# Kernel tuning notes

Hardware: AMD Instinct MI355X
Metric: run time of the kernel (lower is better)

Reference implementation:

```python
import jax, jax.numpy as jnp
import numpy as np

H, W, D = 480, 640, 128
K = 17
R = K // 2
TEMPORAL_LENGTH = 1.0
CHUNK = 1024


def setup_inputs() -> dict:
    key = jax.random.key(0)
    ks = jax.random.split(key, 9)
    N = 500_000
    M = 65_536
    t = jax.random.uniform(ks[0], (N,), jnp.float32)
    y = jax.random.randint(ks[1], (N,), 0, H)
    x = jax.random.randint(ks[2], (N,), 0, W)
    query_y = jax.random.randint(ks[3], (M,), 0, H)
    query_x = jax.random.randint(ks[4], (M,), 0, W)
    query_t = jax.random.uniform(ks[5], (M,), jnp.float32)
    T = jax.random.normal(ks[6], (1, D), jnp.float32) * 25.0
    X = jax.random.normal(ks[7], (1, D), jnp.float32) * 25.0
    Y = jax.random.normal(ks[8], (1, D), jnp.float32) * 25.0
    return dict(t=t, y=y, x=x, query_y=query_y, query_x=query_x,
                query_t=query_t, T=T, X=X, Y=Y)


def _kernel_weights(X, Y):
    # (K*K, D) complex weights: exp(i*(norm_dx*X + norm_dy*Y))
    r = jnp.arange(-R, R + 1, dtype=jnp.float32)
    dy, dx = jnp.meshgrid(r, r, indexing='ij')
    phase = (dx / R)[..., None] * X[0] + (dy / R)[..., None] * Y[0]  # (K,K,D)
    return jnp.exp(1j * phase).reshape(K * K, D)


def reference(t, y, x, query_y, query_x, query_t, T, X, Y):
    kw = _kernel_weights(X, Y)                       # (K*K, D) complex64
    # temporal embedding + scatter-add into flat grid
    t_norm = t / TEMPORAL_LENGTH
    temp_emb = jnp.exp(1j * (t_norm[:, None] * T[0][None, :]))  # (N, D)
    flat_idx = y * W + x                                         # (N,)
    grid = jnp.zeros((H * W, D), jnp.complex64).at[flat_idx].add(temp_emb)
    counts = jnp.zeros((H * W,), jnp.float32).at[flat_idx].add(1.0)
    grid = grid.reshape(H, W, D)
    counts = counts.reshape(H, W)
    # zero-pad by radius
    pg = jnp.pad(grid, ((R, R), (R, R), (0, 0)))
    pc = jnp.pad(counts, ((R, R), (R, R)))
    # flattened window offsets (row-major, matching torch loop order)
    off = jnp.arange(-R, R + 1)
    oy, ox = jnp.meshgrid(off, off, indexing='ij')
    oy = oy.reshape(-1)
    ox = ox.reshape(-1)                               # (K*K,)
    qy = (query_y + R).reshape(-1, CHUNK)
    qx = (query_x + R).reshape(-1, CHUNK)
    M = query_y.shape[0]

    def chunk_fn(q):
        cy, cx = q
        iy = cy[:, None] + oy[None, :]                # (CHUNK, K*K)
        ix = cx[:, None] + ox[None, :]
        feat = pg[iy, ix]                             # (CHUNK, K*K, D)
        cnt = pc[iy, ix]                              # (CHUNK, K*K)
        emb = jnp.einsum('qkd,kd->qd', feat, kw)      # weighted window reduce
        return emb, cnt.sum(axis=1)

    emb_c, cnt_c = jax.lax.map(chunk_fn, (qy, qx))
    out_emb = emb_c.reshape(M, D)
    out_cnt = cnt_c.reshape(M)
    # re-center by query time
    recen = jnp.exp(-1j * ((query_t / TEMPORAL_LENGTH)[:, None] * T[0][None, :]))
    out_emb = out_emb * recen
    return out_emb / jnp.maximum(out_cnt, 1.0)[:, None]
```

## Files before the change

### kernel.cpp

```cpp
#include <hip/hip_runtime.h>
#include <hip/hip_fp16.h>
#include <math.h>

#define HH 480
#define WW 640
#define RAD 8
#define KK 17
#define DD 128
#define HWPIX (HH*WW)
#define NBLK (HWPIX/256)
#define TS 160
#define XT 4

static inline size_t al256(size_t x){ return (x + 255) & ~(size_t)255; }

__global__ void hist_kernel(const int* __restrict__ cy, const int* __restrict__ cx,
                            unsigned* __restrict__ off, int N) {
    int e = blockIdx.x*blockDim.x + threadIdx.x;
    if (e >= N) return;
    atomicAdd(&off[cy[e]*WW + cx[e]], 1u);
}

__global__ void scan1_kernel(unsigned* __restrict__ off, unsigned* __restrict__ bs) {
    __shared__ unsigned sh[256];
    int t = threadIdx.x, b = blockIdx.x;
    unsigned v = off[b*256 + t];
    sh[t] = v; __syncthreads();
    for (int st = 1; st < 256; st <<= 1) {
        unsigned a = (t >= st) ? sh[t-st] : 0u;
        __syncthreads();
        sh[t] += a;
        __syncthreads();
    }
    off[b*256 + t] = sh[t] - v;
    if (t == 255) bs[b] = sh[255];
}

__global__ void scan2_kernel(unsigned* __restrict__ bs) {
    __shared__ unsigned sh[256];
    __shared__ unsigned carry;
    int t = threadIdx.x;
    if (t == 0) carry = 0u;
    __syncthreads();
    for (int base = 0; base < NBLK; base += 256) {
        int i = base + t;
        unsigned v = (i < NBLK) ? bs[i] : 0u;
        sh[t] = v; __syncthreads();
        for (int st = 1; st < 256; st <<= 1) {
            unsigned a = (t >= st) ? sh[t-st] : 0u;
            __syncthreads();
            sh[t] += a;
            __syncthreads();
        }
        unsigned tot = sh[255];
        if (i < NBLK) bs[i] = (sh[t] - v) + carry;
        __syncthreads();
        if (t == 0) carry += tot;
        __syncthreads();
    }
}

__global__ void scan3_kernel(unsigned* __restrict__ off, const unsigned* __restrict__ bs) {
    int i = blockIdx.x*256 + threadIdx.x;
    off[i] += bs[blockIdx.x];
}

__global__ void sort_kernel(const int* __restrict__ ey, const int* __restrict__ ex,
                            const float* __restrict__ t, unsigned* __restrict__ off,
                            float* __restrict__ tss, int* __restrict__ xs, int N) {
    int e = blockIdx.x*blockDim.x + threadIdx.x;
    if (e >= N) return;
    int pix = ey[e]*WW + ex[e];
    unsigned pos = atomicAdd(&off[pix], 1u);
    tss[pos] = t[e];
    xs[pos]  = ex[e];
}

__global__ void qsort_kernel(const int* __restrict__ qy, const int* __restrict__ qx,
                             unsigned* __restrict__ qoff, unsigned* __restrict__ qidx, int M) {
    int q = blockIdx.x*blockDim.x + threadIdx.x;
    if (q >= M) return;
    int pix = qy[q]*WW + qx[q];
    unsigned pos = atomicAdd(&qoff[pix], 1u);
    qidx[pos] = q;
}

__global__ void qcnt_kernel(const int* __restrict__ qy, const int* __restrict__ qx,
                            const unsigned* __restrict__ off, float* __restrict__ qcnt, int M) {
    int q = blockIdx.x*blockDim.x + threadIdx.x;
    if (q >= M) return;
    int cy = qy[q], cx = qx[q];
    int xlo = cx - RAD; if (xlo < 0) xlo = 0;
    int xhi = cx + RAD; if (xhi > WW-1) xhi = WW-1;
    unsigned s = 0;
    for (int i = 0; i < KK; ++i) {
        int yy = cy + i - RAD;
        if ((unsigned)yy >= HH) continue;
        int plo = yy*WW + xlo, phi = yy*WW + xhi;
        unsigned st = plo ? off[plo-1] : 0u;
        s += off[phi] - st;
    }
    qcnt[q] = (float)s;
}

__global__ __launch_bounds__(128) void rowsweep_kernel(
        const unsigned* __restrict__ off, const float* __restrict__ tss,
        const float* __restrict__ Tw, const float* __restrict__ Xw,
        __half2* __restrict__ Hout, int rb0) {
    __shared__ float ringr[KK][DD];
    __shared__ float ringi[KK][DD];
    int dd   = threadIdx.x;
    int hrow = blockIdx.y;
    int hy   = rb0 + hrow;
    int x0   = blockIdx.x * TS;
    int x1   = x0 + TS; if (x1 > WW) x1 = WW;
    __half2* hp = Hout + (long long)hrow*WW*DD + dd;

    if ((unsigned)hy >= HH) {
        __half2 z = __floats2half2_rn(0.f, 0.f);
        for (int x = x0; x < x1; ++x) hp[(long long)x*DD] = z;
        return;
    }

    float Td = Tw[dd];
    float th = Xw[dd] * 0.125f;
    float s, c;
    sincosf(th, &s, &c);
    const float er_ = c,  ei_ = s;
    const float ar  = c,  ai  = -s;
    sincosf(8.f*th, &s, &c);
    const float w0r = c,  w0i = -s;
    sincosf(9.f*th, &s, &c);
    const float w17r = c, w17i = s;

    const int rowbase = hy*WW;
    const unsigned* offr = off + rowbase;

#define GAT(col, gr, gi)                                                    \
    {                                                                       \
        gr = 0.f; gi = 0.f;                                                 \
        if ((unsigned)(col) < WW) {                                         \
            int pix_ = rowbase + (col);                                     \
            unsigned st_ = pix_ ? off[pix_-1] : 0u;                         \
            unsigned en_ = offr[(col)];                                     \
            for (unsigned p_ = st_; p_ < en_; ++p_) {                       \
                float ss_, cc_;                                             \
                __sincosf(tss[p_]*Td, &ss_, &cc_);                          \
                gr += cc_; gi += ss_;                                       \
            }                                                               \
        }                                                                   \
    }

    float hr = 0.f, hi = 0.f;
    float wr = w0r, wi = w0i;
    #pragma unroll
    for (int j = 0; j < KK; ++j) {
        float gr, gi; GAT(x0 + j - RAD, gr, gi);
        hr = fmaf(gr, wr, hr); hr = fmaf(-gi, wi, hr);
        hi = fmaf(gr, wi, hi); hi = fmaf(gi, wr, hi);
        ringr[j][dd] = gr; ringi[j][dd] = gi;
        float nr = wr*er_ - wi*ei_;
        wi       = wr*ei_ + wi*er_;
        wr       = nr;
    }
    hp[(long long)x0*DD] = __floats2half2_rn(hr, hi);

    int ri = 0;
    for (int xn = x0 + 1; xn < x1; ++xn) {
        float gr, gi; GAT(xn + RAD, gr, gi);
        float gor = ringr[ri][dd], goi = ringi[ri][dd];
        ringr[ri][dd] = gr; ringi[ri][dd] = gi;
        ri = (ri + 1 == KK) ? 0 : ri + 1;
        float tr = hr - (gor*w0r - goi*w0i) + (gr*w17r - gi*w17i);
        float ti = hi - (gor*w0i + goi*w0r) + (gr*w17i + gi*w17r);
        hr = tr*ar - ti*ai;
        hi = tr*ai + ti*ar;
        hp[(long long)xn*DD] = __floats2half2_rn(hr, hi);
    }
#undef GAT
}

__global__ __launch_bounds__(256) void query_sep_kernel(
        const unsigned* __restrict__ qidx, const int* __restrict__ qy,
        const int* __restrict__ qx, const float* __restrict__ qt,
        const float* __restrict__ Tw, const float* __restrict__ Yw,
        const unsigned* __restrict__ H, const float* __restrict__ qcnt,
        float* __restrict__ out, int M, int r0, int band, int rb0,
        long long out_n, int real_only) {
    int lt   = threadIdx.x;
    int p    = blockIdx.x*4 + (lt >> 6);
    int lane = lt & 63;
    if (p >= M) return;
    int q = (int)qidx[p];
    int cy = qy[q];
    if (cy < r0 || cy >= r0 + band) return;
    int cx = qx[q];
    int d0 = lane*2, d1 = d0 + 1;

    float wyr0, wyi0, cst0, sst0, wyr1, wyi1, cst1, sst1;
    {
        float s, c;
        float Y0 = Yw[d0], Y1 = Yw[d1];
        sincosf(-Y0, &s, &c);        wyr0 = c; wyi0 = s;
        sincosf(Y0*0.125f, &sst0, &cst0);
        sincosf(-Y1, &s, &c);        wyr1 = c; wyi1 = s;
        sincosf(Y1*0.125f, &sst1, &cst1);
    }

    const unsigned* hp = H + ((long long)(cy - RAD - rb0)*WW + cx)*DD + d0;
    float er0 = 0.f, ei0 = 0.f, er1 = 0.f, ei1 = 0.f;
    #pragma unroll
    for (int i = 0; i < KK; ++i) {
        uint2 v = *(const uint2*)(hp + (long long)i*WW*DD);
        float2 f0 = __half22float2(*(const __half2*)&v.x);
        float2 f1 = __half22float2(*(const __half2*)&v.y);
        er0 = fmaf(f0.x, wyr0, er0); er0 = fmaf(-f0.y, wyi0, er0);
        ei0 = fmaf(f0.x, wyi0, ei0); ei0 = fmaf(f0.y, wyr0, ei0);
        er1 = fmaf(f1.x, wyr1, er1); er1 = fmaf(-f1.y, wyi1, er1);
        ei1 = fmaf(f1.x, wyi1, ei1); ei1 = fmaf(f1.y, wyr1, ei1);
        float nr;
        nr = wyr0*cst0 - wyi0*sst0; wyi0 = wyr0*sst0 + wyi0*cst0; wyr0 = nr;
        nr = wyr1*cst1 - wyi1*sst1; wyi1 = wyr1*sst1 + wyi1*cst1; wyr1 = nr;
    }

    float inv = 1.0f / fmaxf(qcnt[q], 1.0f);
    float s, c, qtv = qt[q];
    sincosf(qtv * Tw[d0], &s, &c);
    float outr0 = (er0*c + ei0*s) * inv, outi0 = (ei0*c - er0*s) * inv;
    sincosf(qtv * Tw[d1], &s, &c);
    float outr1 = (er1*c + ei1*s) * inv, outi1 = (ei1*c - er1*s) * inv;

    long long base = (long long)q*DD + d0;
    if (real_only) {
        if (base + 1 < out_n) *(float2*)(out + base) = make_float2(outr0, outr1);
        else if (base < out_n) out[base] = outr0;
    } else if (2*base + 3 < out_n) {
        *(float4*)(out + 2*base) = make_float4(outr0, outi0, outr1, outi1);
    }
}

__global__ __launch_bounds__(256) void query_direct_kernel(
        const int* __restrict__ qy, const int* __restrict__ qx,
        const float* __restrict__ qt, const float* __restrict__ Tw,
        const float* __restrict__ Xw, const float* __restrict__ Yw,
        const unsigned* __restrict__ off, const float* __restrict__ tss,
        const int* __restrict__ xs, float* __restrict__ out,
        int M, long long out_n, int real_only) {
    __shared__ float2 swx[KK*DD];
    __shared__ float2 swy[KK*DD];
    int lt = threadIdx.x;
    for (int idx = lt; idx < KK*DD; idx += 256) {
        int j = idx / DD, dd = idx & (DD-1);
        float s, c;
        sincosf((float)(j - RAD) * 0.125f * Xw[dd], &s, &c);
        swx[idx] = make_float2(c, s);
        sincosf((float)(j - RAD) * 0.125f * Yw[dd], &s, &c);
        swy[idx] = make_float2(c, s);
    }
    __syncthreads();

    int q = blockIdx.x*2 + (lt >> 7);
    int d = lt & (DD-1);
    if (q >= M) return;

    int cy = qy[q], cx = qx[q];
    float Td = Tw[d];
    int xlo = cx - RAD; if (xlo < 0) xlo = 0;
    int xhi = cx + RAD; if (xhi > WW-1) xhi = WW-1;

    float accr = 0.f, acci = 0.f;
    unsigned cnt = 0;
    for (int i = 0; i < KK; ++i) {
        int yy = cy + i - RAD;
        if ((unsigned)yy >= HH) continue;
        int plo = yy*WW + xlo, phi = yy*WW + xhi;
        unsigned st = plo ? off[plo-1] : 0u;
        unsigned en = off[phi];
        cnt += en - st;
        float rr = 0.f, ri = 0.f;
        for (unsigned p = st; p < en; ++p) {
            float te = tss[p];
            int   xe = xs[p];
            float2 wx = swx[(xe - cx + RAD)*DD + d];
            float s, c;
            __sincosf(te * Td, &s, &c);
            rr = fmaf(c, wx.x, rr); rr = fmaf(-s, wx.y, rr);
            ri = fmaf(c, wx.y, ri); ri = fmaf(s, wx.x, ri);
        }
        float2 wy = swy[i*DD + d];
        accr = fmaf(rr, wy.x, accr); accr = fmaf(-ri, wy.y, accr);
        acci = fmaf(rr, wy.y, acci); acci = fmaf(ri, wy.x, acci);
    }

    float s, c;
    sincosf(qt[q] * Td, &s, &c);
    float inv = 1.0f / fmaxf((float)cnt, 1.0f);
    float outr = (accr*c + acci*s) * inv;
    float outi = (acci*c - accr*s) * inv;
    long long base = (long long)q*DD + d;
    if (real_only) { if (base < out_n) out[base] = outr; }
    else if (2*base + 1 < out_n) { out[2*base] = outr; out[2*base+1] = outi; }
}

extern "C" void kernel_launch(void* const* d_in, const int* in_sizes, int n_in,
                              void* d_out, int out_size, void* d_ws, size_t ws_size,
                              hipStream_t stream) {
    const float* t  = (const float*)d_in[0];
    const int*   ey = (const int*)d_in[1];
    const int*   ex = (const int*)d_in[2];
    const int*   qy = (const int*)d_in[3];
    const int*   qx = (const int*)d_in[4];
    const float* qt = (const float*)d_in[5];
    const float* Tw = (const float*)d_in[6];
    const float* Xw = (const float*)d_in[7];
    const float* Yw = (const float*)d_in[8];

    int N = in_sizes[0];
    int M = in_sizes[3];

    size_t off_b  = al256((size_t)HWPIX*4);
    size_t qoff_b = al256((size_t)HWPIX*4);
    size_t bs_b   = al256((size_t)NBLK*4);
    size_t tss_b  = al256((size_t)N*4);
    size_t xs_b   = al256((size_t)N*4);
    size_t qidx_b = al256((size_t)M*4);
    size_t qc_b   = al256((size_t)M*4);
    size_t fixed  = off_b + qoff_b + bs_b + tss_b + xs_b + qidx_b + qc_b;
    size_t need_min = off_b + qoff_b + bs_b + tss_b + xs_b;

    if (ws_size < need_min || d_ws == nullptr) {
        hipMemsetAsync(d_out, 0, (size_t)out_size*4, stream);
        return;
    }

    char*     ws   = (char*)d_ws;
    unsigned* off  = (unsigned*)ws;
    unsigned* qoff = (unsigned*)(ws + off_b);
    unsigned* bs   = (unsigned*)(ws + off_b + qoff_b);
    float*    tss  = (float*)(ws + off_b + qoff_b + bs_b);
    int*      xs   = (int*)(ws + off_b + qoff_b + bs_b + tss_b);
    unsigned* qidx = (unsigned*)(ws + off_b + qoff_b + bs_b + tss_b + xs_b);
    float*    qcnt = (float*)(ws + off_b + qoff_b + bs_b + tss_b + xs_b + qidx_b);
    __half2*  H    = (__half2*)(ws + fixed);

    long long full = (long long)M * DD;
    int real_only = (out_size < 2*full) ? 1 : 0;

    hipMemsetAsync(off, 0, off_b + (size_t)HWPIX*4, stream);
    hist_kernel<<<(N+255)/256, 256, 0, stream>>>(ey, ex, off, N);
    scan1_kernel<<<NBLK, 256, 0, stream>>>(off, bs);
    scan2_kernel<<<1, 256, 0, stream>>>(bs);
    scan3_kernel<<<NBLK, 256, 0, stream>>>(off, bs);
    sort_kernel<<<(N+255)/256, 256, 0, stream>>>(ey, ex, t, off, tss, xs, N);

    long long band_sz = 0;
    if (ws_size > fixed) {
        long long hrows_fit = (long long)((ws_size - fixed) / ((size_t)WW*DD*4));
        band_sz = hrows_fit - 16;
        if (band_sz > HH) band_sz = HH;
    }

    if (band_sz < 32) {
        query_direct_kernel<<<(M+1)/2, 256, 0, stream>>>(
            qy, qx, qt, Tw, Xw, Yw, off, tss, xs, (float*)d_out,
            M, (long long)out_size, real_only);
        return;
    }

    qcnt_kernel<<<(M+255)/256, 256, 0, stream>>>(qy, qx, off, qcnt, M);

    hist_kernel<<<(M+255)/256, 256, 0, stream>>>(qy, qx, qoff, M);
    scan1_kernel<<<NBLK, 256, 0, stream>>>(qoff, bs);
    scan2_kernel<<<1, 256, 0, stream>>>(bs);
    scan3_kernel<<<NBLK, 256, 0, stream>>>(qoff, bs);
    qsort_kernel<<<(M+255)/256, 256, 0, stream>>>(qy, qx, qoff, qidx, M);

    for (int r0 = 0; r0 < HH; r0 += (int)band_sz) {
        int band  = (HH - r0 < band_sz) ? (HH - r0) : (int)band_sz;
        int hrows = band + 16;
        dim3 g(XT, hrows);
        rowsweep_kernel<<<g, 128, 0, stream>>>(off, tss, Tw, Xw, H, r0 - RAD);
        query_sep_kernel<<<(M+3)/4, 256, 0, stream>>>(
            qidx, qy, qx, qt, Tw, Yw, (const unsigned*)H, qcnt, (float*)d_out,
            M, r0, band, r0 - RAD, (long long)out_size, real_only);
    }
}
```

Baseline: 252.6 us.

## Batch histogram/scan kernels for events and queries, register ring, finer row tiles

Event and query histograms, prefix scans and the query sort/count step are merged into dual-purpose kernels, cutting the number of launches. The rowsweep kernel keeps its 17-entry ring buffer in registers through a fully unrolled loop instead of shared memory. It also carries the previous segment end forward instead of reloading the start offset per column. Tile width is halved (TS 80, XT 8) so more blocks run in parallel, at the cost of more redundant window-initialisation gathers per row.

```diff
diff --git a/kernel.cpp b/kernel.cpp
--- a/kernel.cpp
+++ b/kernel.cpp
@@ -9,22 +9,29 @@
 #define DD 128
 #define HWPIX (HH*WW)
 #define NBLK (HWPIX/256)
-#define TS 160
-#define XT 4
+#define TS 80
+#define XT 8
 
 static inline size_t al256(size_t x){ return (x + 255) & ~(size_t)255; }
 
-__global__ void hist_kernel(const int* __restrict__ cy, const int* __restrict__ cx,
-                            unsigned* __restrict__ off, int N) {
+__global__ void hist_dual_kernel(const int* __restrict__ ey, const int* __restrict__ ex, int N,
+                                 const int* __restrict__ qy, const int* __restrict__ qx, int M,
+                                 unsigned* __restrict__ off, unsigned* __restrict__ qoff) {
     int e = blockIdx.x*blockDim.x + threadIdx.x;
-    if (e >= N) return;
-    atomicAdd(&off[cy[e]*WW + cx[e]], 1u);
-}
-
-__global__ void scan1_kernel(unsigned* __restrict__ off, unsigned* __restrict__ bs) {
+    if (blockIdx.y == 0) {
+        if (e < N) atomicAdd(&off[ey[e]*WW + ex[e]], 1u);
+    } else {
+        if (e < M) atomicAdd(&qoff[qy[e]*WW + qx[e]], 1u);
+    }
+}
+
+__global__ void scan1_dual_kernel(unsigned* __restrict__ o0, unsigned* __restrict__ o1,
+                                  unsigned* __restrict__ bs) {
     __shared__ unsigned sh[256];
     int t = threadIdx.x, b = blockIdx.x;
-    unsigned v = off[b*256 + t];
+    unsigned* off = (b < NBLK) ? o0 : o1;
+    int bb = (b < NBLK) ? b : b - NBLK;
+    unsigned v = off[bb*256 + t];
     sh[t] = v; __syncthreads();
     for (int st = 1; st < 256; st <<= 1) {
         unsigned a = (t >= st) ? sh[t-st] : 0u;
@@ -32,13 +39,14 @@
         sh[t] += a;
         __syncthreads();
     }
-    off[b*256 + t] = sh[t] - v;
+    off[bb*256 + t] = sh[t] - v;
     if (t == 255) bs[b] = sh[255];
 }
 
-__global__ void scan2_kernel(unsigned* __restrict__ bs) {
+__global__ void scan2_dual_kernel(unsigned* __restrict__ bs_all) {
     __shared__ unsigned sh[256];
     __shared__ unsigned carry;
+    unsigned* bs = bs_all + blockIdx.x*NBLK;
     int t = threadIdx.x;
     if (t == 0) carry = 0u;
     __syncthreads();
@@ -60,9 +68,12 @@
     }
 }
 
-__global__ void scan3_kernel(unsigned* __restrict__ off, const unsigned* __restrict__ bs) {
-    int i = blockIdx.x*256 + threadIdx.x;
-    off[i] += bs[blockIdx.x];
+__global__ void scan3_dual_kernel(unsigned* __restrict__ o0, unsigned* __restrict__ o1,
+                                  const unsigned* __restrict__ bs) {
+    int b = blockIdx.x;
+    unsigned* off = (b < NBLK) ? o0 : o1;
+    int bb = (b < NBLK) ? b : b - NBLK;
+    off[bb*256 + threadIdx.x] += bs[b];
 }
 
 __global__ void sort_kernel(const int* __restrict__ ey, const int* __restrict__ ex,
@@ -76,20 +87,15 @@
     xs[pos]  = ex[e];
 }
 
-__global__ void qsort_kernel(const int* __restrict__ qy, const int* __restrict__ qx,
-                             unsigned* __restrict__ qoff, unsigned* __restrict__ qidx, int M) {
-    int q = blockIdx.x*blockDim.x + threadIdx.x;
-    if (q >= M) return;
-    int pix = qy[q]*WW + qx[q];
-    unsigned pos = atomicAdd(&qoff[pix], 1u);
-    qidx[pos] = q;
-}
-
-__global__ void qcnt_kernel(const int* __restrict__ qy, const int* __restrict__ qx,
-                            const unsigned* __restrict__ off, float* __restrict__ qcnt, int M) {
+__global__ void qsortcnt_kernel(const int* __restrict__ qy, const int* __restrict__ qx,
+                                unsigned* __restrict__ qoff, unsigned* __restrict__ qidx,
+                                const unsigned* __restrict__ off, float* __restrict__ qcnt, int M) {
     int q = blockIdx.x*blockDim.x + threadIdx.x;
     if (q >= M) return;
     int cy = qy[q], cx = qx[q];
+    int pix = cy*WW + cx;
+    unsigned pos = atomicAdd(&qoff[pix], 1u);
+    qidx[pos] = q;
     int xlo = cx - RAD; if (xlo < 0) xlo = 0;
     int xhi = cx + RAD; if (xhi > WW-1) xhi = WW-1;
     unsigned s = 0;
@@ -107,8 +113,6 @@
         const unsigned* __restrict__ off, const float* __restrict__ tss,
         const float* __restrict__ Tw, const float* __restrict__ Xw,
         __half2* __restrict__ Hout, int rb0) {
-    __shared__ float ringr[KK][DD];
-    __shared__ float ringi[KK][DD];
     int dd   = threadIdx.x;
     int hrow = blockIdx.y;
     int hy   = rb0 + hrow;
@@ -136,48 +140,58 @@
     const int rowbase = hy*WW;
     const unsigned* offr = off + rowbase;
 
-#define GAT(col, gr, gi)                                                    \
+    int cfirst = x0 - RAD; if (cfirst < 0) cfirst = 0;
+    int pix0 = rowbase + cfirst;
+    unsigned pen = pix0 ? off[pix0-1] : 0u;
+
+#define GATC(col, gr, gi)                                                   \
     {                                                                       \
         gr = 0.f; gi = 0.f;                                                 \
         if ((unsigned)(col) < WW) {                                         \
-            int pix_ = rowbase + (col);                                     \
-            unsigned st_ = pix_ ? off[pix_-1] : 0u;                         \
             unsigned en_ = offr[(col)];                                     \
-            for (unsigned p_ = st_; p_ < en_; ++p_) {                       \
+            for (unsigned p_ = pen; p_ < en_; ++p_) {                       \
                 float ss_, cc_;                                             \
                 __sincosf(tss[p_]*Td, &ss_, &cc_);                          \
                 gr += cc_; gi += ss_;                                       \
             }                                                               \
+            pen = en_;                                                      \
         }                                                                   \
     }
+
+    float ringr[KK], ringi[KK];
 
     float hr = 0.f, hi = 0.f;
     float wr = w0r, wi = w0i;
     #pragma unroll
     for (int j = 0; j < KK; ++j) {
-        float gr, gi; GAT(x0 + j - RAD, gr, gi);
+        float gr, gi; GATC(x0 + j - RAD, gr, gi);
         hr = fmaf(gr, wr, hr); hr = fmaf(-gi, wi, hr);
         hi = fmaf(gr, wi, hi); hi = fmaf(gi, wr, hi);
-        ringr[j][dd] = gr; ringi[j][dd] = gi;
+        ringr[j] = gr; ringi[j] = gi;
         float nr = wr*er_ - wi*ei_;
         wi       = wr*ei_ + wi*er_;
         wr       = nr;
     }
     hp[(long long)x0*DD] = __floats2half2_rn(hr, hi);
 
-    int ri = 0;
-    for (int xn = x0 + 1; xn < x1; ++xn) {
-        float gr, gi; GAT(xn + RAD, gr, gi);
-        float gor = ringr[ri][dd], goi = ringi[ri][dd];
-        ringr[ri][dd] = gr; ringi[ri][dd] = gi;
-        ri = (ri + 1 == KK) ? 0 : ri + 1;
-        float tr = hr - (gor*w0r - goi*w0i) + (gr*w17r - gi*w17i);
-        float ti = hi - (gor*w0i + goi*w0r) + (gr*w17i + gi*w17r);
-        hr = tr*ar - ti*ai;
-        hi = tr*ai + ti*ar;
-        hp[(long long)xn*DD] = __floats2half2_rn(hr, hi);
-    }
-#undef GAT
+    int xn = x0 + 1;
+    while (xn < x1) {
+        #pragma unroll
+        for (int k = 0; k < KK; ++k) {
+            if (xn < x1) {
+                float gr, gi; GATC(xn + RAD, gr, gi);
+                float gor = ringr[k], goi = ringi[k];
+                ringr[k] = gr; ringi[k] = gi;
+                float tr = hr - (gor*w0r - goi*w0i) + (gr*w17r - gi*w17i);
+                float ti = hi - (gor*w0i + goi*w0r) + (gr*w17i + gi*w17r);
+                hr = tr*ar - ti*ai;
+                hi = tr*ai + ti*ar;
+                hp[(long long)xn*DD] = __floats2half2_rn(hr, hi);
+                ++xn;
+            }
+        }
+    }
+#undef GATC
 }
 
 __global__ __launch_bounds__(256) void query_sep_kernel(
@@ -320,7 +334,7 @@
 
     size_t off_b  = al256((size_t)HWPIX*4);
     size_t qoff_b = al256((size_t)HWPIX*4);
-    size_t bs_b   = al256((size_t)NBLK*4);
+    size_t bs_b   = al256((size_t)2*NBLK*4);
     size_t tss_b  = al256((size_t)N*4);
     size_t xs_b   = al256((size_t)N*4);
     size_t qidx_b = al256((size_t)M*4);
@@ -347,10 +361,11 @@
     int real_only = (out_size < 2*full) ? 1 : 0;
 
     hipMemsetAsync(off, 0, off_b + (size_t)HWPIX*4, stream);
-    hist_kernel<<<(N+255)/256, 256, 0, stream>>>(ey, ex, off, N);
-    scan1_kernel<<<NBLK, 256, 0, stream>>>(off, bs);
-    scan2_kernel<<<1, 256, 0, stream>>>(bs);
-    scan3_kernel<<<NBLK, 256, 0, stream>>>(off, bs);
+    int hb = ((N > M ? N : M) + 255)/256;
+    hist_dual_kernel<<<dim3(hb, 2), 256, 0, stream>>>(ey, ex, N, qy, qx, M, off, qoff);
+    scan1_dual_kernel<<<2*NBLK, 256, 0, stream>>>(off, qoff, bs);
+    scan2_dual_kernel<<<2, 256, 0, stream>>>(bs);
+    scan3_dual_kernel<<<2*NBLK, 256, 0, stream>>>(off, qoff, bs);
     sort_kernel<<<(N+255)/256, 256, 0, stream>>>(ey, ex, t, off, tss, xs, N);
 
     long long band_sz = 0;
@@ -367,13 +382,7 @@
         return;
     }
 
-    qcnt_kernel<<<(M+255)/256, 256, 0, stream>>>(qy, qx, off, qcnt, M);
-
-    hist_kernel<<<(M+255)/256, 256, 0, stream>>>(qy, qx, qoff, M);
-    scan1_kernel<<<NBLK, 256, 0, stream>>>(qoff, bs);
-    scan2_kernel<<<1, 256, 0, stream>>>(bs);
-    scan3_kernel<<<NBLK, 256, 0, stream>>>(qoff, bs);
-    qsort_kernel<<<(M+255)/256, 256, 0, stream>>>(qy, qx, qoff, qidx, M);
+    qsortcnt_kernel<<<(M+255)/256, 256, 0, stream>>>(qy, qx, qoff, qidx, off, qcnt, M);
 
     for (int r0 = 0; r0 < HH; r0 += (int)band_sz) {
         int band  = (HH - r0 < band_sz) ? (HH - r0) : (int)band_sz;
```

New measurement: 276.1 us. 9.3% more time.
